# Kernel optimization log

Hardware: AMD Instinct MI355X
Metric: run time of the kernel (lower is better)

The kernel has to match this reference:

```python
import jax, jax.numpy as jnp
import numpy as np

N = 50000
E = 800000
D = 128
LN_EPS = 1e-5


def setup_inputs() -> dict:
    key = jax.random.key(0)
    k1, k2, k3, k4 = jax.random.split(key, 4)
    x = jax.random.normal(k1, (N, D), dtype=jnp.float32)
    edge_index = jax.random.randint(k2, (2, E), 0, N, dtype=jnp.int32)
    # xavier_uniform with gain=sqrt(2) (relu gain)
    gain = float(np.sqrt(2.0))
    lim_lin = gain * float(np.sqrt(6.0 / (D + D)))
    W_lin = jax.random.uniform(k3, (D, D), dtype=jnp.float32, minval=-lim_lin, maxval=lim_lin)
    lim_attn = gain * float(np.sqrt(6.0 / (2 * D + 1)))
    W_attn = jax.random.uniform(k4, (1, 2 * D), dtype=jnp.float32, minval=-lim_attn, maxval=lim_attn)
    ln_scale = jnp.ones((D,), dtype=jnp.float32)
    ln_bias = jnp.zeros((D,), dtype=jnp.float32)
    return {"x": x, "W_lin": W_lin, "W_attn": W_attn,
            "ln_scale": ln_scale, "ln_bias": ln_bias, "edge_index": edge_index}


def _layer_norm(h, scale, bias):
    mu = jnp.mean(h, axis=-1, keepdims=True)
    var = jnp.mean(jnp.square(h - mu), axis=-1, keepdims=True)
    return (h - mu) * jax.lax.rsqrt(var + LN_EPS) * scale + bias


def reference(x, W_lin, W_attn, ln_scale, ln_bias, edge_index):
    n = x.shape[0]
    src, dst = edge_index[0], edge_index[1]
    # h = x @ W_lin^T  [N, D]
    h = jnp.einsum('nd,od->no', x, W_lin)
    # attention score: [h_src || h_dst] @ W_attn^T == h_src@a_src + h_dst@a_dst
    d = h.shape[1]
    a_src = W_attn[0, :d]
    a_dst = W_attn[0, d:]
    s_src = h @ a_src  # [N]
    s_dst = h @ a_dst  # [N]
    scores = s_src[src] + s_dst[dst]  # [E]
    scores = jnp.where(scores >= 0, scores, 0.2 * scores)  # leaky_relu(0.2)
    # segment softmax over edges grouped by dst
    seg_max = jax.ops.segment_max(scores, dst, num_segments=n)  # [N]
    seg_max = jnp.where(jnp.isfinite(seg_max), seg_max, 0.0)
    ex = jnp.exp(scores - seg_max[dst])  # [E]
    denom = jax.ops.segment_sum(ex, dst, num_segments=n)  # [N]
    alpha = ex / jnp.where(denom > 0, denom, 1.0)[dst]  # [E]
    # weighted message aggregation (dropout is identity in eval mode)
    msgs = h[src] * alpha[:, None]  # [E, D]
    agg = jax.ops.segment_sum(msgs, dst, num_segments=n)  # [N, D]
    # residual (input_dim == output_dim -> no projection) + layer norm
    return _layer_norm(agg + x, ln_scale, ln_bias)
```

## Files before the change

kernel.cpp:

```cpp
#include <hip/hip_runtime.h>

#define N_NODES 50000
#define E_EDGES 800000
#define D_DIM   128
#define LN_EPS  1e-5f
#define BCAP    64
#define PREP_BLOCKS 196
#define GEMM_BLOCKS 391
#define HIST_BLOCKS 782
#define SCAT_BLOCKS 782
#define GATH_BLOCKS 12500

typedef __bf16 bf16x8 __attribute__((ext_vector_type(8)));
typedef unsigned short ushort8v __attribute__((ext_vector_type(8)));
typedef float f32x4 __attribute__((ext_vector_type(4)));
typedef int i32x2v __attribute__((ext_vector_type(2)));
typedef int i32x16v __attribute__((ext_vector_type(16)));

__device__ inline unsigned short f2b(float f) {
    unsigned int u = __float_as_uint(f);
    unsigned int r = u + 0x7FFFu + ((u >> 16) & 1u);
    return (unsigned short)(r >> 16);
}
__device__ inline float b2f(unsigned short h) {
    return __uint_as_float((unsigned int)h << 16);
}
__device__ inline float blo(unsigned int u) { return __uint_as_float(u << 16); }
__device__ inline float bhi(unsigned int u) { return __uint_as_float(u & 0xFFFF0000u); }

__device__ inline i32x16v sload16(const uint2* p) {
    i32x16v r;
    asm volatile("s_load_dwordx16 %0, %1, 0x0\n\ts_waitcnt lgkmcnt(0)"
                 : "=&s"(r) : "s"(p));
    return r;
}
__device__ inline i32x2v sload2(const uint2* p) {
    i32x2v r;
    asm volatile("s_load_dwordx2 %0, %1, 0x0\n\ts_waitcnt lgkmcnt(0)"
                 : "=&s"(r) : "s"(p));
    return r;
}

__global__ void k_prep(const float* __restrict__ W,
                       unsigned short* __restrict__ Whp,
                       unsigned short* __restrict__ Wlp,
                       int* __restrict__ count) {
    int i = blockIdx.x * 256 + threadIdx.x;
    if (i < N_NODES) count[i] = 0;
    if (i < 16384) {
        int o = i >> 7, k = i & 127;
        float v = W[i];
        unsigned short h = f2b(v);
        unsigned short l = f2b(v - b2f(h));
        int idx = (k >> 3) * 1024 + o * 8 + (k & 7);
        Whp[idx] = h;
        Wlp[idx] = l;
    }
}

__global__ __launch_bounds__(256, 2) void k_gemm_hist(
        const float* __restrict__ xin, const unsigned short* __restrict__ Wpk,
        const float* __restrict__ Wa, const int* __restrict__ dst,
        int* __restrict__ count, int* __restrict__ erank,
        unsigned short* __restrict__ hb,
        float* __restrict__ ssrc, float* __restrict__ sdst) {
    __shared__ float4 wl4[4096];
    const int tid = threadIdx.x;

    if (blockIdx.x >= GEMM_BLOCKS) {
        int e0 = (blockIdx.x - GEMM_BLOCKS) * 1024 + tid * 4;
        if (e0 < E_EDGES) {
            int4 dv = *(const int4*)&dst[e0];
            int r0 = atomicAdd(&count[dv.x], 1);
            int r1 = atomicAdd(&count[dv.y], 1);
            int r2 = atomicAdd(&count[dv.z], 1);
            int r3 = atomicAdd(&count[dv.w], 1);
            *(int4*)&erank[e0] = make_int4(r0, r1, r2, r3);
        }
        return;
    }

    {
        const float4* wsrc = (const float4*)Wpk;
        #pragma unroll
        for (int i = 0; i < 16; ++i)
            wl4[i * 256 + tid] = wsrc[i * 256 + tid];
    }

    const int c = tid & 15;
    const int g = (tid >> 4) & 3;
    const int w = tid >> 6;
    const int n0 = blockIdx.x * 128;

    bf16x8 ah[2][4], al[2][4];
    #pragma unroll
    for (int t = 0; t < 2; ++t) {
        int n = n0 + w * 32 + t * 16 + c;
        if (n > N_NODES - 1) n = N_NODES - 1;
        const float* xr = xin + (size_t)n * 128;
        #pragma unroll
        for (int s = 0; s < 4; ++s) {
            float4 f0 = *(const float4*)(xr + s * 32 + g * 8);
            float4 f1 = *(const float4*)(xr + s * 32 + g * 8 + 4);
            float fv[8] = {f0.x, f0.y, f0.z, f0.w, f1.x, f1.y, f1.z, f1.w};
            ushort8v uh, ul;
            #pragma unroll
            for (int j = 0; j < 8; ++j) {
                unsigned short hj = f2b(fv[j]);
                uh[j] = hj;
                ul[j] = f2b(fv[j] - b2f(hj));
            }
            ah[t][s] = __builtin_bit_cast(bf16x8, uh);
            al[t][s] = __builtin_bit_cast(bf16x8, ul);
        }
    }

    __syncthreads();
    const bf16x8* wb = (const bf16x8*)wl4;

    f32x4 acc[2][8];
    #pragma unroll
    for (int t = 0; t < 2; ++t)
        #pragma unroll
        for (int cb = 0; cb < 8; ++cb)
            acc[t][cb] = (f32x4){0.f, 0.f, 0.f, 0.f};

    #pragma unroll
    for (int cb = 0; cb < 8; ++cb) {
        #pragma unroll
        for (int s = 0; s < 4; ++s) {
            int q = (s * 4 + g) * 128 + cb * 16 + c;
            bf16x8 bh = wb[q];
            bf16x8 bl = wb[2048 + q];
            acc[0][cb] = __builtin_amdgcn_mfma_f32_16x16x32_bf16(ah[0][s], bh, acc[0][cb], 0, 0, 0);
            acc[1][cb] = __builtin_amdgcn_mfma_f32_16x16x32_bf16(ah[1][s], bh, acc[1][cb], 0, 0, 0);
            acc[0][cb] = __builtin_amdgcn_mfma_f32_16x16x32_bf16(al[0][s], bh, acc[0][cb], 0, 0, 0);
            acc[1][cb] = __builtin_amdgcn_mfma_f32_16x16x32_bf16(al[1][s], bh, acc[1][cb], 0, 0, 0);
            acc[0][cb] = __builtin_amdgcn_mfma_f32_16x16x32_bf16(ah[0][s], bl, acc[0][cb], 0, 0, 0);
            acc[1][cb] = __builtin_amdgcn_mfma_f32_16x16x32_bf16(ah[1][s], bl, acc[1][cb], 0, 0, 0);
        }
    }

    float asv[8], adv[8];
    #pragma unroll
    for (int cb = 0; cb < 8; ++cb) {
        asv[cb] = Wa[cb * 16 + c];
        adv[cb] = Wa[128 + cb * 16 + c];
    }
    #pragma unroll
    for (int t = 0; t < 2; ++t) {
        #pragma unroll
        for (int i = 0; i < 4; ++i) {
            int n = n0 + w * 32 + t * 16 + g * 4 + i;
            float ps = 0.f, pd = 0.f;
            #pragma unroll
            for (int cb = 0; cb < 8; ++cb) {
                float v = acc[t][cb][i];
                ps += v * asv[cb];
                pd += v * adv[cb];
            }
            #pragma unroll
            for (int off = 1; off < 16; off <<= 1) {
                ps += __shfl_xor(ps, off);
                pd += __shfl_xor(pd, off);
            }
            if (c == 0 && n < N_NODES) { ssrc[n] = ps; sdst[n] = pd; }
        }
    }

    __syncthreads();
    unsigned short* hlds = (unsigned short*)wl4;
    #pragma unroll
    for (int t = 0; t < 2; ++t)
        #pragma unroll
        for (int cb = 0; cb < 8; ++cb)
            #pragma unroll
            for (int i = 0; i < 4; ++i)
                hlds[(w * 32 + t * 16 + g * 4 + i) * 128 + cb * 16 + c] =
                    f2b(acc[t][cb][i]);
    __syncthreads();
    #pragma unroll
    for (int ii = 0; ii < 8; ++ii) {
        int cidx = ii * 256 + tid;
        int row = cidx >> 4, off = cidx & 15;
        int n = n0 + row;
        if (n < N_NODES) {
            ushort8v v = *(const ushort8v*)&hlds[row * 128 + off * 8];
            *(ushort8v*)&hb[(size_t)n * 128 + off * 8] = v;
        }
    }
}

__global__ __launch_bounds__(256) void k_scatter(
        const int* __restrict__ src, const int* __restrict__ dst,
        const int* __restrict__ erank,
        const float* __restrict__ ssrc, const float* __restrict__ sdst,
        uint2* __restrict__ sev) {
    int e0 = (blockIdx.x * 256 + threadIdx.x) * 4;
    if (e0 >= E_EDGES) return;
    int4 sv = *(const int4*)&src[e0];
    int4 dv = *(const int4*)&dst[e0];
    int4 rk = *(const int4*)&erank[e0];
    float ss0 = ssrc[sv.x], ss1 = ssrc[sv.y], ss2 = ssrc[sv.z], ss3 = ssrc[sv.w];
    float sd0 = sdst[dv.x], sd1 = sdst[dv.y], sd2 = sdst[dv.z], sd3 = sdst[dv.w];
    float c0 = ss0 + sd0, c1 = ss1 + sd1, c2 = ss2 + sd2, c3 = ss3 + sd3;
    c0 = c0 >= 0.f ? c0 : 0.2f * c0;
    c1 = c1 >= 0.f ? c1 : 0.2f * c1;
    c2 = c2 >= 0.f ? c2 : 0.2f * c2;
    c3 = c3 >= 0.f ? c3 : 0.2f * c3;
    if (rk.x < BCAP) sev[(size_t)dv.x * BCAP + rk.x] = make_uint2((unsigned int)sv.x, __float_as_uint(__expf(c0)));
    if (rk.y < BCAP) sev[(size_t)dv.y * BCAP + rk.y] = make_uint2((unsigned int)sv.y, __float_as_uint(__expf(c1)));
    if (rk.z < BCAP) sev[(size_t)dv.z * BCAP + rk.z] = make_uint2((unsigned int)sv.z, __float_as_uint(__expf(c2)));
    if (rk.w < BCAP) sev[(size_t)dv.w * BCAP + rk.w] = make_uint2((unsigned int)sv.w, __float_as_uint(__expf(c3)));
}

__global__ __launch_bounds__(256) void k_gather(
        const int* __restrict__ count,
        const uint2* __restrict__ sev,
        const unsigned short* __restrict__ hb, const float* __restrict__ x,
        const float* __restrict__ scale, const float* __restrict__ bias,
        float* __restrict__ out) {
    int n    = __builtin_amdgcn_readfirstlane(blockIdx.x * 4 + (threadIdx.x >> 6));
    int lane = threadIdx.x & 63;
    int deg = count[n]; if (deg > BCAP) deg = BCAP;
    int beg = n * BCAP;
    int end = beg + deg;
    const unsigned int* hb32 = (const unsigned int*)hb;

    float a0 = 0.f, a1 = 0.f, b0 = 0.f, b1 = 0.f, den = 0.f, den2 = 0.f;

    int i = beg;
    for (; i + 15 < end; i += 16) {
        int ib = __builtin_amdgcn_readfirstlane(i);
        i32x16v s0 = sload16(sev + ib);
        i32x16v s1 = sload16(sev + ib + 8);
        unsigned int u[16];
        #pragma unroll
        for (int q = 0; q < 8; ++q)
            u[q] = hb32[(((unsigned)s0[2 * q]) << 6) + lane];
        #pragma unroll
        for (int q = 0; q < 8; ++q)
            u[8 + q] = hb32[(((unsigned)s1[2 * q]) << 6) + lane];
        #pragma unroll
        for (int q = 0; q < 8; q += 2) {
            float ex0 = __uint_as_float(s0[2 * q + 1]);
            float ex1 = __uint_as_float(s0[2 * q + 3]);
            den  += ex0; den2 += ex1;
            a0 += ex0 * blo(u[q]);     a1 += ex0 * bhi(u[q]);
            b0 += ex1 * blo(u[q + 1]); b1 += ex1 * bhi(u[q + 1]);
        }
        #pragma unroll
        for (int q = 0; q < 8; q += 2) {
            float ex0 = __uint_as_float(s1[2 * q + 1]);
            float ex1 = __uint_as_float(s1[2 * q + 3]);
            den  += ex0; den2 += ex1;
            a0 += ex0 * blo(u[8 + q]);     a1 += ex0 * bhi(u[8 + q]);
            b0 += ex1 * blo(u[8 + q + 1]); b1 += ex1 * bhi(u[8 + q + 1]);
        }
    }
    for (; i + 7 < end; i += 8) {
        int ib = __builtin_amdgcn_readfirstlane(i);
        i32x16v s0 = sload16(sev + ib);
        unsigned int u[8];
        #pragma unroll
        for (int q = 0; q < 8; ++q)
            u[q] = hb32[(((unsigned)s0[2 * q]) << 6) + lane];
        #pragma unroll
        for (int q = 0; q < 8; q += 2) {
            float ex0 = __uint_as_float(s0[2 * q + 1]);
            float ex1 = __uint_as_float(s0[2 * q + 3]);
            den  += ex0; den2 += ex1;
            a0 += ex0 * blo(u[q]);     a1 += ex0 * bhi(u[q]);
            b0 += ex1 * blo(u[q + 1]); b1 += ex1 * bhi(u[q + 1]);
        }
    }
    for (; i < end; ++i) {
        i32x2v p2 = sload2(sev + __builtin_amdgcn_readfirstlane(i));
        unsigned int u0 = hb32[(((unsigned)p2[0]) << 6) + lane];
        float ex0 = __uint_as_float(p2[1]);
        den += ex0;
        a0 += ex0 * blo(u0);
        a1 += ex0 * bhi(u0);
    }
    a0 += b0; a1 += b1; den += den2;

    float inv_d = 1.f / (den > 0.f ? den : 1.f);
    size_t base = (size_t)n * 128 + 2 * lane;
    float2 xv = *(const float2*)&x[base];
    float r0 = a0 * inv_d + xv.x;
    float r1 = a1 * inv_d + xv.y;

    float sum = r0 + r1;
    #pragma unroll
    for (int off = 32; off >= 1; off >>= 1) sum += __shfl_xor(sum, off);
    float mu = sum * (1.f / 128.f);
    float d0 = r0 - mu, d1 = r1 - mu;
    float ss = d0 * d0 + d1 * d1;
    #pragma unroll
    for (int off = 32; off >= 1; off >>= 1) ss += __shfl_xor(ss, off);
    float inv = rsqrtf(ss * (1.f / 128.f) + LN_EPS);
    float o0 = d0 * inv * scale[2 * lane]     + bias[2 * lane];
    float o1 = d1 * inv * scale[2 * lane + 1] + bias[2 * lane + 1];
    *(float2*)&out[base] = make_float2(o0, o1);
}

extern "C" void kernel_launch(void* const* d_in, const int* in_sizes, int n_in,
                              void* d_out, int out_size, void* d_ws, size_t ws_size,
                              hipStream_t stream) {
    const float* x        = (const float*)d_in[0];
    const float* W_lin    = (const float*)d_in[1];
    const float* W_attn   = (const float*)d_in[2];
    const float* ln_scale = (const float*)d_in[3];
    const float* ln_bias  = (const float*)d_in[4];
    const int*   edge     = (const int*)d_in[5];
    const int*   e_src    = edge;
    const int*   e_dst    = edge + E_EDGES;
    float* out = (float*)d_out;

    char* ws = (char*)d_ws;
    unsigned short* hb  = (unsigned short*)(ws);
    unsigned short* Whp = (unsigned short*)(ws + 12800000);
    unsigned short* Wlp = (unsigned short*)(ws + 12832768);
    float* ssrc   = (float*)(ws + 12865536);
    float* sdst   = (float*)(ws + 13065536);
    int*   count  = (int*)  (ws + 13265536);
    uint2* sev    = (uint2*)(ws + 13465536);
    int*   erank  = (int*)  (ws + 39065536);

    k_prep     <<<PREP_BLOCKS, 256, 0, stream>>>(W_lin, Whp, Wlp, count);
    k_gemm_hist<<<GEMM_BLOCKS + HIST_BLOCKS, 256, 0, stream>>>(
                    x, Whp, W_attn, e_dst, count, erank, hb, ssrc, sdst);
    k_scatter  <<<SCAT_BLOCKS, 256, 0, stream>>>(e_src, e_dst, erank, ssrc, sdst, sev);
    k_gather   <<<GATH_BLOCKS, 256, 0, stream>>>(count, sev, hb, x,
                                                 ln_scale, ln_bias, out);
}
```

Measured before the change: 175.0 us.

## Fold attention vector into weights to compute scores from x, fuse scatter

The attention projections are precomputed as p = W_lin^T a in the prep kernel. A new k_score kernel then computes per-node src/dst scores directly from x, which no longer depend on the GEMM output. This lets the histogram blocks compute scores and write the edge buckets inline, removing the separate scatter kernel and the erank buffer round-trip. The cost is an extra pass reading x (25.6 MB) and a new launch, and the score math now runs in full fp32 rather than through the bf16-split GEMM result, which changes the order of rounding.

```diff
diff --git a/kernel.cpp b/kernel.cpp
--- a/kernel.cpp
+++ b/kernel.cpp
@@ -5,10 +5,10 @@
 #define D_DIM   128
 #define LN_EPS  1e-5f
 #define BCAP    64
-#define PREP_BLOCKS 196
+#define PREP_BLOCKS 197
 #define GEMM_BLOCKS 391
 #define HIST_BLOCKS 782
-#define SCAT_BLOCKS 782
+#define SCORE_BLOCKS 12500
 #define GATH_BLOCKS 12500
 
 typedef __bf16 bf16x8 __attribute__((ext_vector_type(8)));
@@ -41,11 +41,12 @@
     return r;
 }
 
-__global__ void k_prep(const float* __restrict__ W,
+__global__ void k_prep(const float* __restrict__ W, const float* __restrict__ Wa,
                        unsigned short* __restrict__ Whp,
                        unsigned short* __restrict__ Wlp,
-                       int* __restrict__ count) {
-    int i = blockIdx.x * 256 + threadIdx.x;
+                       int* __restrict__ count, float* __restrict__ p) {
+    int tid = threadIdx.x;
+    int i = blockIdx.x * 256 + tid;
     if (i < N_NODES) count[i] = 0;
     if (i < 16384) {
         int o = i >> 7, k = i & 127;
@@ -56,26 +57,64 @@
         Whp[idx] = h;
         Wlp[idx] = l;
     }
-}
-
-__global__ __launch_bounds__(256, 2) void k_gemm_hist(
+    if (blockIdx.x == 196) {
+        int which = tid >> 7;
+        int k = tid & 127;
+        float acc = 0.f;
+        #pragma unroll 8
+        for (int o = 0; o < 128; ++o)
+            acc += W[o * 128 + k] * Wa[which * 128 + o];
+        p[which * 128 + k] = acc;
+    }
+}
+
+__global__ __launch_bounds__(256) void k_score(
+        const float* __restrict__ x, const float* __restrict__ p,
+        float* __restrict__ ssrc, float* __restrict__ sdst) {
+    int n    = blockIdx.x * 4 + (threadIdx.x >> 6);
+    int lane = threadIdx.x & 63;
+    float2 xv = *(const float2*)&x[(size_t)n * 128 + 2 * lane];
+    float2 ps = *(const float2*)&p[2 * lane];
+    float2 pd = *(const float2*)&p[128 + 2 * lane];
+    float s = xv.x * ps.x + xv.y * ps.y;
+    float d = xv.x * pd.x + xv.y * pd.y;
+    #pragma unroll
+    for (int off = 32; off >= 1; off >>= 1) {
+        s += __shfl_xor(s, off);
+        d += __shfl_xor(d, off);
+    }
+    if (lane == 0) { ssrc[n] = s; sdst[n] = d; }
+}
+
+__global__ __launch_bounds__(256, 2) void k_gemm_hsct(
         const float* __restrict__ xin, const unsigned short* __restrict__ Wpk,
-        const float* __restrict__ Wa, const int* __restrict__ dst,
-        int* __restrict__ count, int* __restrict__ erank,
-        unsigned short* __restrict__ hb,
-        float* __restrict__ ssrc, float* __restrict__ sdst) {
+        const int* __restrict__ src, const int* __restrict__ dst,
+        const float* __restrict__ ssrc, const float* __restrict__ sdst,
+        int* __restrict__ count, unsigned short* __restrict__ hb,
+        uint2* __restrict__ sev) {
     __shared__ float4 wl4[4096];
     const int tid = threadIdx.x;
 
     if (blockIdx.x >= GEMM_BLOCKS) {
         int e0 = (blockIdx.x - GEMM_BLOCKS) * 1024 + tid * 4;
         if (e0 < E_EDGES) {
+            int4 sv = *(const int4*)&src[e0];
             int4 dv = *(const int4*)&dst[e0];
+            float ss0 = ssrc[sv.x], ss1 = ssrc[sv.y], ss2 = ssrc[sv.z], ss3 = ssrc[sv.w];
+            float sd0 = sdst[dv.x], sd1 = sdst[dv.y], sd2 = sdst[dv.z], sd3 = sdst[dv.w];
             int r0 = atomicAdd(&count[dv.x], 1);
             int r1 = atomicAdd(&count[dv.y], 1);
             int r2 = atomicAdd(&count[dv.z], 1);
             int r3 = atomicAdd(&count[dv.w], 1);
-            *(int4*)&erank[e0] = make_int4(r0, r1, r2, r3);
+            float c0 = ss0 + sd0, c1 = ss1 + sd1, c2 = ss2 + sd2, c3 = ss3 + sd3;
+            c0 = c0 >= 0.f ? c0 : 0.2f * c0;
+            c1 = c1 >= 0.f ? c1 : 0.2f * c1;
+            c2 = c2 >= 0.f ? c2 : 0.2f * c2;
+            c3 = c3 >= 0.f ? c3 : 0.2f * c3;
+            if (r0 < BCAP) sev[(size_t)dv.x * BCAP + r0] = make_uint2((unsigned int)sv.x, __float_as_uint(__expf(c0)));
+            if (r1 < BCAP) sev[(size_t)dv.y * BCAP + r1] = make_uint2((unsigned int)sv.y, __float_as_uint(__expf(c1)));
+            if (r2 < BCAP) sev[(size_t)dv.z * BCAP + r2] = make_uint2((unsigned int)sv.z, __float_as_uint(__expf(c2)));
+            if (r3 < BCAP) sev[(size_t)dv.w * BCAP + r3] = make_uint2((unsigned int)sv.w, __float_as_uint(__expf(c3)));
         }
         return;
     }
@@ -141,33 +180,6 @@
         }
     }
 
-    float asv[8], adv[8];
-    #pragma unroll
-    for (int cb = 0; cb < 8; ++cb) {
-        asv[cb] = Wa[cb * 16 + c];
-        adv[cb] = Wa[128 + cb * 16 + c];
-    }
-    #pragma unroll
-    for (int t = 0; t < 2; ++t) {
-        #pragma unroll
-        for (int i = 0; i < 4; ++i) {
-            int n = n0 + w * 32 + t * 16 + g * 4 + i;
-            float ps = 0.f, pd = 0.f;
-            #pragma unroll
-            for (int cb = 0; cb < 8; ++cb) {
-                float v = acc[t][cb][i];
-                ps += v * asv[cb];
-                pd += v * adv[cb];
-            }
-            #pragma unroll
-            for (int off = 1; off < 16; off <<= 1) {
-                ps += __shfl_xor(ps, off);
-                pd += __shfl_xor(pd, off);
-            }
-            if (c == 0 && n < N_NODES) { ssrc[n] = ps; sdst[n] = pd; }
-        }
-    }
-
     __syncthreads();
     unsigned short* hlds = (unsigned short*)wl4;
     #pragma unroll
@@ -189,29 +201,6 @@
             *(ushort8v*)&hb[(size_t)n * 128 + off * 8] = v;
         }
     }
-}
-
-__global__ __launch_bounds__(256) void k_scatter(
-        const int* __restrict__ src, const int* __restrict__ dst,
-        const int* __restrict__ erank,
-        const float* __restrict__ ssrc, const float* __restrict__ sdst,
-        uint2* __restrict__ sev) {
-    int e0 = (blockIdx.x * 256 + threadIdx.x) * 4;
-    if (e0 >= E_EDGES) return;
-    int4 sv = *(const int4*)&src[e0];
-    int4 dv = *(const int4*)&dst[e0];
-    int4 rk = *(const int4*)&erank[e0];
-    float ss0 = ssrc[sv.x], ss1 = ssrc[sv.y], ss2 = ssrc[sv.z], ss3 = ssrc[sv.w];
-    float sd0 = sdst[dv.x], sd1 = sdst[dv.y], sd2 = sdst[dv.z], sd3 = sdst[dv.w];
-    float c0 = ss0 + sd0, c1 = ss1 + sd1, c2 = ss2 + sd2, c3 = ss3 + sd3;
-    c0 = c0 >= 0.f ? c0 : 0.2f * c0;
-    c1 = c1 >= 0.f ? c1 : 0.2f * c1;
-    c2 = c2 >= 0.f ? c2 : 0.2f * c2;
-    c3 = c3 >= 0.f ? c3 : 0.2f * c3;
-    if (rk.x < BCAP) sev[(size_t)dv.x * BCAP + rk.x] = make_uint2((unsigned int)sv.x, __float_as_uint(__expf(c0)));
-    if (rk.y < BCAP) sev[(size_t)dv.y * BCAP + rk.y] = make_uint2((unsigned int)sv.y, __float_as_uint(__expf(c1)));
-    if (rk.z < BCAP) sev[(size_t)dv.z * BCAP + rk.z] = make_uint2((unsigned int)sv.z, __float_as_uint(__expf(c2)));
-    if (rk.w < BCAP) sev[(size_t)dv.w * BCAP + rk.w] = make_uint2((unsigned int)sv.w, __float_as_uint(__expf(c3)));
 }
 
 __global__ __launch_bounds__(256) void k_gather(
@@ -325,12 +314,12 @@
     float* sdst   = (float*)(ws + 13065536);
     int*   count  = (int*)  (ws + 13265536);
     uint2* sev    = (uint2*)(ws + 13465536);
-    int*   erank  = (int*)  (ws + 39065536);
-
-    k_prep     <<<PREP_BLOCKS, 256, 0, stream>>>(W_lin, Whp, Wlp, count);
-    k_gemm_hist<<<GEMM_BLOCKS + HIST_BLOCKS, 256, 0, stream>>>(
-                    x, Whp, W_attn, e_dst, count, erank, hb, ssrc, sdst);
-    k_scatter  <<<SCAT_BLOCKS, 256, 0, stream>>>(e_src, e_dst, erank, ssrc, sdst, sev);
+    float* p      = (float*)(ws + 39065536);
+
+    k_prep     <<<PREP_BLOCKS, 256, 0, stream>>>(W_lin, W_attn, Whp, Wlp, count, p);
+    k_score    <<<SCORE_BLOCKS, 256, 0, stream>>>(x, p, ssrc, sdst);
+    k_gemm_hsct<<<GEMM_BLOCKS + HIST_BLOCKS, 256, 0, stream>>>(
+                    x, Whp, e_src, e_dst, ssrc, sdst, count, hb, sev);
     k_gather   <<<GATH_BLOCKS, 256, 0, stream>>>(count, sev, hb, x,
                                                  ln_scale, ln_bias, out);
 }
```

After: 179.9 us. 2.8% more time.

## Fuse edge bucketing into histogram pass and compute attention scores in gather

Applied to the files above, without the earlier changes.

The separate scatter kernel is removed. The histogram blocks now write the source index straight into the per-destination bucket using the atomic rank, so the erank buffer is no longer needed. The gather kernel computes leaky-relu and exp itself from ssrc and sdst instead of reading precomputed exp values, which halves the bucket entry size and saves a kernel launch plus an E-sized round trip. In exchange, gather does an extra per-lane ssrc load and exp for every edge, and the bucket writes now run in the same pass as the GEMM.

```diff
diff --git a/kernel.cpp b/kernel.cpp
--- a/kernel.cpp
+++ b/kernel.cpp
@@ -8,13 +8,12 @@
 #define PREP_BLOCKS 196
 #define GEMM_BLOCKS 391
 #define HIST_BLOCKS 782
-#define SCAT_BLOCKS 782
 #define GATH_BLOCKS 12500
 
 typedef __bf16 bf16x8 __attribute__((ext_vector_type(8)));
 typedef unsigned short ushort8v __attribute__((ext_vector_type(8)));
 typedef float f32x4 __attribute__((ext_vector_type(4)));
-typedef int i32x2v __attribute__((ext_vector_type(2)));
+typedef int i32x8v __attribute__((ext_vector_type(8)));
 typedef int i32x16v __attribute__((ext_vector_type(16)));
 
 __device__ inline unsigned short f2b(float f) {
@@ -28,15 +27,21 @@
 __device__ inline float blo(unsigned int u) { return __uint_as_float(u << 16); }
 __device__ inline float bhi(unsigned int u) { return __uint_as_float(u & 0xFFFF0000u); }
 
-__device__ inline i32x16v sload16(const uint2* p) {
+__device__ inline i32x16v sload16(const unsigned int* p) {
     i32x16v r;
     asm volatile("s_load_dwordx16 %0, %1, 0x0\n\ts_waitcnt lgkmcnt(0)"
                  : "=&s"(r) : "s"(p));
     return r;
 }
-__device__ inline i32x2v sload2(const uint2* p) {
-    i32x2v r;
-    asm volatile("s_load_dwordx2 %0, %1, 0x0\n\ts_waitcnt lgkmcnt(0)"
+__device__ inline i32x8v sload8(const unsigned int* p) {
+    i32x8v r;
+    asm volatile("s_load_dwordx8 %0, %1, 0x0\n\ts_waitcnt lgkmcnt(0)"
+                 : "=&s"(r) : "s"(p));
+    return r;
+}
+__device__ inline int sload1(const unsigned int* p) {
+    int r;
+    asm volatile("s_load_dword %0, %1, 0x0\n\ts_waitcnt lgkmcnt(0)"
                  : "=&s"(r) : "s"(p));
     return r;
 }
@@ -60,8 +65,9 @@
 
 __global__ __launch_bounds__(256, 2) void k_gemm_hist(
         const float* __restrict__ xin, const unsigned short* __restrict__ Wpk,
-        const float* __restrict__ Wa, const int* __restrict__ dst,
-        int* __restrict__ count, int* __restrict__ erank,
+        const float* __restrict__ Wa,
+        const int* __restrict__ src, const int* __restrict__ dst,
+        int* __restrict__ count, unsigned int* __restrict__ sev,
         unsigned short* __restrict__ hb,
         float* __restrict__ ssrc, float* __restrict__ sdst) {
     __shared__ float4 wl4[4096];
@@ -70,12 +76,16 @@
     if (blockIdx.x >= GEMM_BLOCKS) {
         int e0 = (blockIdx.x - GEMM_BLOCKS) * 1024 + tid * 4;
         if (e0 < E_EDGES) {
+            int4 sv = *(const int4*)&src[e0];
             int4 dv = *(const int4*)&dst[e0];
             int r0 = atomicAdd(&count[dv.x], 1);
             int r1 = atomicAdd(&count[dv.y], 1);
             int r2 = atomicAdd(&count[dv.z], 1);
             int r3 = atomicAdd(&count[dv.w], 1);
-            *(int4*)&erank[e0] = make_int4(r0, r1, r2, r3);
+            if (r0 < BCAP) sev[dv.x * BCAP + r0] = (unsigned int)sv.x;
+            if (r1 < BCAP) sev[dv.y * BCAP + r1] = (unsigned int)sv.y;
+            if (r2 < BCAP) sev[dv.z * BCAP + r2] = (unsigned int)sv.z;
+            if (r3 < BCAP) sev[dv.w * BCAP + r3] = (unsigned int)sv.w;
         }
         return;
     }
@@ -191,33 +201,12 @@
     }
 }
 
-__global__ __launch_bounds__(256) void k_scatter(
-        const int* __restrict__ src, const int* __restrict__ dst,
-        const int* __restrict__ erank,
-        const float* __restrict__ ssrc, const float* __restrict__ sdst,
-        uint2* __restrict__ sev) {
-    int e0 = (blockIdx.x * 256 + threadIdx.x) * 4;
-    if (e0 >= E_EDGES) return;
-    int4 sv = *(const int4*)&src[e0];
-    int4 dv = *(const int4*)&dst[e0];
-    int4 rk = *(const int4*)&erank[e0];
-    float ss0 = ssrc[sv.x], ss1 = ssrc[sv.y], ss2 = ssrc[sv.z], ss3 = ssrc[sv.w];
-    float sd0 = sdst[dv.x], sd1 = sdst[dv.y], sd2 = sdst[dv.z], sd3 = sdst[dv.w];
-    float c0 = ss0 + sd0, c1 = ss1 + sd1, c2 = ss2 + sd2, c3 = ss3 + sd3;
-    c0 = c0 >= 0.f ? c0 : 0.2f * c0;
-    c1 = c1 >= 0.f ? c1 : 0.2f * c1;
-    c2 = c2 >= 0.f ? c2 : 0.2f * c2;
-    c3 = c3 >= 0.f ? c3 : 0.2f * c3;
-    if (rk.x < BCAP) sev[(size_t)dv.x * BCAP + rk.x] = make_uint2((unsigned int)sv.x, __float_as_uint(__expf(c0)));
-    if (rk.y < BCAP) sev[(size_t)dv.y * BCAP + rk.y] = make_uint2((unsigned int)sv.y, __float_as_uint(__expf(c1)));
-    if (rk.z < BCAP) sev[(size_t)dv.z * BCAP + rk.z] = make_uint2((unsigned int)sv.z, __float_as_uint(__expf(c2)));
-    if (rk.w < BCAP) sev[(size_t)dv.w * BCAP + rk.w] = make_uint2((unsigned int)sv.w, __float_as_uint(__expf(c3)));
-}
-
 __global__ __launch_bounds__(256) void k_gather(
         const int* __restrict__ count,
-        const uint2* __restrict__ sev,
-        const unsigned short* __restrict__ hb, const float* __restrict__ x,
+        const unsigned int* __restrict__ sev,
+        const unsigned short* __restrict__ hb,
+        const float* __restrict__ ssrc, const float* __restrict__ sdst,
+        const float* __restrict__ x,
         const float* __restrict__ scale, const float* __restrict__ bias,
         float* __restrict__ out) {
     int n    = __builtin_amdgcn_readfirstlane(blockIdx.x * 4 + (threadIdx.x >> 6));
@@ -226,6 +215,7 @@
     int beg = n * BCAP;
     int end = beg + deg;
     const unsigned int* hb32 = (const unsigned int*)hb;
+    const float sdn = sdst[n];
 
     float a0 = 0.f, a1 = 0.f, b0 = 0.f, b1 = 0.f, den = 0.f, den2 = 0.f;
 
@@ -233,51 +223,47 @@
     for (; i + 15 < end; i += 16) {
         int ib = __builtin_amdgcn_readfirstlane(i);
         i32x16v s0 = sload16(sev + ib);
-        i32x16v s1 = sload16(sev + ib + 8);
         unsigned int u[16];
         #pragma unroll
-        for (int q = 0; q < 8; ++q)
-            u[q] = hb32[(((unsigned)s0[2 * q]) << 6) + lane];
-        #pragma unroll
-        for (int q = 0; q < 8; ++q)
-            u[8 + q] = hb32[(((unsigned)s1[2 * q]) << 6) + lane];
-        #pragma unroll
-        for (int q = 0; q < 8; q += 2) {
-            float ex0 = __uint_as_float(s0[2 * q + 1]);
-            float ex1 = __uint_as_float(s0[2 * q + 3]);
+        for (int q = 0; q < 16; ++q)
+            u[q] = hb32[(((unsigned)s0[q]) << 6) + lane];
+        #pragma unroll
+        for (int q = 0; q < 16; q += 2) {
+            float sc0 = ssrc[(unsigned)s0[q]]     + sdn;
+            float sc1 = ssrc[(unsigned)s0[q + 1]] + sdn;
+            sc0 = sc0 >= 0.f ? sc0 : 0.2f * sc0;
+            sc1 = sc1 >= 0.f ? sc1 : 0.2f * sc1;
+            float ex0 = __expf(sc0), ex1 = __expf(sc1);
             den  += ex0; den2 += ex1;
             a0 += ex0 * blo(u[q]);     a1 += ex0 * bhi(u[q]);
             b0 += ex1 * blo(u[q + 1]); b1 += ex1 * bhi(u[q + 1]);
         }
-        #pragma unroll
-        for (int q = 0; q < 8; q += 2) {
-            float ex0 = __uint_as_float(s1[2 * q + 1]);
-            float ex1 = __uint_as_float(s1[2 * q + 3]);
-            den  += ex0; den2 += ex1;
-            a0 += ex0 * blo(u[8 + q]);     a1 += ex0 * bhi(u[8 + q]);
-            b0 += ex1 * blo(u[8 + q + 1]); b1 += ex1 * bhi(u[8 + q + 1]);
-        }
     }
     for (; i + 7 < end; i += 8) {
         int ib = __builtin_amdgcn_readfirstlane(i);
-        i32x16v s0 = sload16(sev + ib);
+        i32x8v s0 = sload8(sev + ib);
         unsigned int u[8];
         #pragma unroll
         for (int q = 0; q < 8; ++q)
-            u[q] = hb32[(((unsigned)s0[2 * q]) << 6) + lane];
+            u[q] = hb32[(((unsigned)s0[q]) << 6) + lane];
         #pragma unroll
         for (int q = 0; q < 8; q += 2) {
-            float ex0 = __uint_as_float(s0[2 * q + 1]);
-            float ex1 = __uint_as_float(s0[2 * q + 3]);
+            float sc0 = ssrc[(unsigned)s0[q]]     + sdn;
+            float sc1 = ssrc[(unsigned)s0[q + 1]] + sdn;
+            sc0 = sc0 >= 0.f ? sc0 : 0.2f * sc0;
+            sc1 = sc1 >= 0.f ? sc1 : 0.2f * sc1;
+            float ex0 = __expf(sc0), ex1 = __expf(sc1);
             den  += ex0; den2 += ex1;
             a0 += ex0 * blo(u[q]);     a1 += ex0 * bhi(u[q]);
             b0 += ex1 * blo(u[q + 1]); b1 += ex1 * bhi(u[q + 1]);
         }
     }
     for (; i < end; ++i) {
-        i32x2v p2 = sload2(sev + __builtin_amdgcn_readfirstlane(i));
-        unsigned int u0 = hb32[(((unsigned)p2[0]) << 6) + lane];
-        float ex0 = __uint_as_float(p2[1]);
+        int s = sload1(sev + __builtin_amdgcn_readfirstlane(i));
+        unsigned int u0 = hb32[(((unsigned)s) << 6) + lane];
+        float sc = ssrc[(unsigned)s] + sdn;
+        sc = sc >= 0.f ? sc : 0.2f * sc;
+        float ex0 = __expf(sc);
         den += ex0;
         a0 += ex0 * blo(u0);
         a1 += ex0 * bhi(u0);
@@ -324,13 +310,11 @@
     float* ssrc   = (float*)(ws + 12865536);
     float* sdst   = (float*)(ws + 13065536);
     int*   count  = (int*)  (ws + 13265536);
-    uint2* sev    = (uint2*)(ws + 13465536);
-    int*   erank  = (int*)  (ws + 39065536);
+    unsigned int* sev = (unsigned int*)(ws + 13465536);
 
     k_prep     <<<PREP_BLOCKS, 256, 0, stream>>>(W_lin, Whp, Wlp, count);
     k_gemm_hist<<<GEMM_BLOCKS + HIST_BLOCKS, 256, 0, stream>>>(
-                    x, Whp, W_attn, e_dst, count, erank, hb, ssrc, sdst);
-    k_scatter  <<<SCAT_BLOCKS, 256, 0, stream>>>(e_src, e_dst, erank, ssrc, sdst, sev);
-    k_gather   <<<GATH_BLOCKS, 256, 0, stream>>>(count, sev, hb, x,
+                    x, Whp, W_attn, e_src, e_dst, count, sev, hb, ssrc, sdst);
+    k_gather   <<<GATH_BLOCKS, 256, 0, stream>>>(count, sev, hb, ssrc, sdst, x,
                                                  ln_scale, ln_bias, out);
 }
```

Result: no change. 177.8 us (+1.6%).
